# Performance work log

Measured on AMD Instinct MI355X. Metric: run time of the kernel, lower is better.

Reference implementation:

```python
import jax, jax.numpy as jnp
import numpy as np

DIM = 1536
NH = 12
HD = DIM // NH  # 128
B = 1
F, H, W = 8, 16, 16
S = F * H * W  # 2048
EPS = 1e-6
MAX_POS = 1024


def _rmsnorm(x, g):
    # WanRMSNorm: x * rsqrt(mean(x^2, -1) + eps) * weight  (computed in fp32)
    return x * jax.lax.rsqrt(jnp.mean(x * x, axis=-1, keepdims=True) + EPS) * g


def _rope_apply(x, grid_sizes, freqs):
    # x: [B, S, NH, HD]; freqs: [1024, HD//2] angles. Full (level-0) freqs_i path.
    f, h, w = [int(v) for v in np.asarray(grid_sizes[0])]
    c = HD // 2  # 64
    s0 = c - 2 * (c // 3)  # 22 (frame freqs)
    s1 = c // 3            # 21 (height / width freqs)
    p0 = freqs[:f, :s0]
    p1 = freqs[:h, s0:s0 + s1]
    p2 = freqs[:w, s0 + s1:]
    ang = jnp.concatenate([
        jnp.broadcast_to(p0[:, None, None, :], (f, h, w, s0)),
        jnp.broadcast_to(p1[None, :, None, :], (f, h, w, s1)),
        jnp.broadcast_to(p2[None, None, :, :], (f, h, w, s1)),
    ], axis=-1).reshape(f * h * w, 1, c)  # [S, 1, c]
    cos, sin = jnp.cos(ang), jnp.sin(ang)
    xr = x[0].reshape(S, NH, c, 2)  # pairs -> complex rotation
    x0, x1 = xr[..., 0], xr[..., 1]
    out = jnp.stack([x0 * cos - x1 * sin, x0 * sin + x1 * cos], axis=-1)
    return out.reshape(S, NH, HD)[None].astype(jnp.float32)  # [1, S, NH, HD]


def setup_inputs() -> dict:
    key = jax.random.key(0)
    ks = jax.random.split(key, 8)
    sc = 0.02
    return {
        "x": jax.random.normal(ks[0], (B, S, DIM), jnp.float32),
        "freqs": jax.random.uniform(ks[1], (MAX_POS, HD // 2), jnp.float32, 0.0, 2.0 * np.pi),
        "wq": jax.random.normal(ks[2], (DIM, DIM), jnp.float32) * sc,
        "bq": jnp.zeros((DIM,), jnp.float32),
        "wk": jax.random.normal(ks[3], (DIM, DIM), jnp.float32) * sc,
        "bk": jnp.zeros((DIM,), jnp.float32),
        "wv": jax.random.normal(ks[4], (DIM, DIM), jnp.float32) * sc,
        "bv": jnp.zeros((DIM,), jnp.float32),
        "wo": jax.random.normal(ks[5], (DIM, DIM), jnp.float32) * sc,
        "bo": jnp.zeros((DIM,), jnp.float32),
        "gq": jnp.ones((DIM,), jnp.float32),
        "gk": jnp.ones((DIM,), jnp.float32),
        "seq_lens": jnp.array([S], jnp.int32),
        "grid_sizes": jnp.array([[F, H, W]], jnp.int32),
    }


def reference(x, freqs, wq, bq, wk, bk, wv, bv, wo, bo, gq, gk, seq_lens, grid_sizes):
    b, s = x.shape[:2]
    q = _rmsnorm(x @ wq.T + bq, gq).reshape(b, s, NH, HD)
    k = _rmsnorm(x @ wk.T + bk, gk).reshape(b, s, NH, HD)
    v = (x @ wv.T + bv).reshape(b, s, NH, HD)
    q = _rope_apply(q, grid_sizes, freqs)
    k = _rope_apply(k, grid_sizes, freqs)
    # flash_attention with k_lens=seq_lens, full window -> masked SDPA
    kmask = jnp.arange(s)[None, :] < seq_lens[:, None]  # [b, s]
    scores = jnp.einsum('bqnd,bknd->bnqk', q, k) / np.sqrt(HD).astype(np.float32)
    scores = jnp.where(kmask[:, None, None, :], scores, jnp.finfo(scores.dtype).min)
    attn = jax.nn.softmax(scores, axis=-1)
    out = jnp.einsum('bnqk,bknd->bqnd', attn, v).reshape(b, s, DIM)
    return out @ wo.T + bo
```

## Files before the change

### kernel.cpp

```cpp
#include <hip/hip_runtime.h>
#include <math.h>

#define DIMN 1536
#define NHEAD 12
#define HDIM 128
#define SLEN 2048
#define EPSV 1e-6f

typedef __attribute__((ext_vector_type(8))) short short8;
typedef __attribute__((ext_vector_type(4))) short short4v;
typedef __attribute__((ext_vector_type(4))) float f32x4;

typedef __attribute__((address_space(1))) const void gvoid_t;
typedef __attribute__((address_space(3))) void lvoid_t;

__device__ __forceinline__ void gload_lds16(const void* g, void* l) {
    __builtin_amdgcn_global_load_lds((gvoid_t*)g, (lvoid_t*)l, 16, 0, 0);
}

__device__ inline short to_bf16(float f) {
    union { float f; unsigned u; } v; v.f = f;
    unsigned r = (v.u + 0x7FFFu + ((v.u >> 16) & 1u)) >> 16;
    return (short)r;
}
__device__ inline float bf_to_f(short h) {
    union { unsigned u; float f; } v;
    v.u = ((unsigned)(unsigned short)h) << 16;
    return v.f;
}

__device__ __forceinline__ int swz8(int row, int c) {
    return c ^ (row & 7);
}

__global__ __launch_bounds__(256)
void cast5(const float* s0, const float* s1, const float* s2,
           const float* s3, const float* s4,
           short* d0, short* d1, short* d2, short* d3, short* d4,
           int n0, int nw)
{
    const float* s; short* d; int n;
    switch (blockIdx.y) {
        case 0: s = s0; d = d0; n = n0; break;
        case 1: s = s1; d = d1; n = nw; break;
        case 2: s = s2; d = d2; n = nw; break;
        case 3: s = s3; d = d3; n = nw; break;
        default: s = s4; d = d4; n = nw; break;
    }
    int idx = (blockIdx.x * 256 + threadIdx.x) * 8;
    if (idx >= n) return;
    float4 a = *(const float4*)(s + idx);
    float4 b = *(const float4*)(s + idx + 4);
    short8 r;
    r[0] = to_bf16(a.x); r[1] = to_bf16(a.y); r[2] = to_bf16(a.z); r[3] = to_bf16(a.w);
    r[4] = to_bf16(b.x); r[5] = to_bf16(b.y); r[6] = to_bf16(b.z); r[7] = to_bf16(b.w);
    *(short8*)(d + idx) = r;
}

__device__ __forceinline__ void gemm_mainloop(const short* __restrict__ A,
    const short* __restrict__ W, int m0, int n0, int K,
    short* As, short* Bs, f32x4 (&acc)[4][4])
{
    const int tid = threadIdx.x;
    const int wave = tid >> 6, lane = tid & 63;
    const int quad = lane >> 4, col = lane & 15;
    const int wm = wave >> 1, wn = wave & 1;
    const int sr = tid >> 3;
    const int sc = tid & 7;

    for (int kt = 0; kt < K; kt += 64) {
        __syncthreads();
        #pragma unroll
        for (int i = 0; i < 4; ++i) {
            const int row = i * 32 + sr;
            const int c = swz8(row, sc);
            gload_lds16(A + (size_t)(m0 + row) * K + kt + c * 8, As + i * 2048 + tid * 8);
        }
        #pragma unroll
        for (int i = 0; i < 4; ++i) {
            const int row = i * 32 + sr;
            const int c = swz8(row, sc);
            gload_lds16(W + (size_t)(n0 + row) * K + kt + c * 8, Bs + i * 2048 + tid * 8);
        }
        __syncthreads();

        #pragma unroll
        for (int kb = 0; kb < 2; ++kb) {
            short8 af[4], bf[4];
            #pragma unroll
            for (int mt = 0; mt < 4; ++mt) {
                const int row = wm * 64 + mt * 16 + col;
                af[mt] = *(const short8*)&As[row * 64 + swz8(row, kb * 4 + quad) * 8];
            }
            #pragma unroll
            for (int nt = 0; nt < 4; ++nt) {
                const int row = wn * 64 + nt * 16 + col;
                bf[nt] = *(const short8*)&Bs[row * 64 + swz8(row, kb * 4 + quad) * 8];
            }
            #pragma unroll
            for (int mt = 0; mt < 4; ++mt)
                #pragma unroll
                for (int nt = 0; nt < 4; ++nt)
                    acc[mt][nt] = __builtin_amdgcn_mfma_f32_16x16x32_bf16(
                        af[mt], bf[nt], acc[mt][nt], 0, 0, 0);
        }
    }
}

__global__ __launch_bounds__(256)
void gemm_qkv(const short* __restrict__ A,
              const short* __restrict__ W0, const short* __restrict__ W1,
              const short* __restrict__ W2,
              const float* __restrict__ b0, const float* __restrict__ b1,
              const float* __restrict__ b2,
              short* __restrict__ Y0, short* __restrict__ Y1,
              short* __restrict__ Vp)
{
    __shared__ __attribute__((aligned(16))) short As[128 * 64];
    __shared__ __attribute__((aligned(16))) short Bs[128 * 64];

    const int sel = blockIdx.x / (DIMN / 128);
    const int nb  = blockIdx.x % (DIMN / 128);
    const short* W    = (sel == 0) ? W0 : (sel == 1) ? W1 : W2;
    const float* bias = (sel == 0) ? b0 : (sel == 1) ? b1 : b2;

    const int tid = threadIdx.x;
    const int wave = tid >> 6, lane = tid & 63;
    const int quad = lane >> 4, col = lane & 15;
    const int wm = wave >> 1, wn = wave & 1;
    const int m0 = blockIdx.y * 128, n0 = nb * 128;

    f32x4 acc[4][4];
    #pragma unroll
    for (int i = 0; i < 4; ++i)
        #pragma unroll
        for (int j = 0; j < 4; ++j)
            #pragma unroll
            for (int r = 0; r < 4; ++r) acc[i][j][r] = 0.f;

    gemm_mainloop(A, W, m0, n0, DIMN, As, Bs, acc);

    if (sel < 2) {
        short* Y = (sel == 0) ? Y0 : Y1;
        #pragma unroll
        for (int mt = 0; mt < 4; ++mt) {
            #pragma unroll
            for (int nt = 0; nt < 4; ++nt) {
                const int n = n0 + wn * 64 + nt * 16 + col;
                const float bb = bias[n];
                #pragma unroll
                for (int r = 0; r < 4; ++r) {
                    const int m = m0 + wm * 64 + mt * 16 + quad * 4 + r;
                    Y[(size_t)m * DIMN + n] = to_bf16(acc[mt][nt][r] + bb);
                }
            }
        }
    } else {
        const int head = nb;
        const int kt64 = blockIdx.y * 2 + wm;
        #pragma unroll
        for (int mt = 0; mt < 4; ++mt) {
            #pragma unroll
            for (int nt = 0; nt < 4; ++nt) {
                const int n = n0 + wn * 64 + nt * 16 + col;
                const float bb = bias[n];
                const int dt = wn * 4 + nt;
                const int chunk = (head * 64 + kt64 * 2 + (mt >> 1)) * 8 + dt;
                const int off = ((mt & 1) * 2 + (quad >> 1)) * 128 + col * 8 + (quad & 1) * 4;
                short4v o;
                #pragma unroll
                for (int r = 0; r < 4; ++r) o[r] = to_bf16(acc[mt][nt][r] + bb);
                *(short4v*)(Vp + (size_t)chunk * 512 + off) = o;
            }
        }
    }
}

__global__ __launch_bounds__(256)
void gemm_out(const short* __restrict__ A, const short* __restrict__ W,
              const float* __restrict__ bias, float* __restrict__ Yf)
{
    __shared__ __attribute__((aligned(16))) short As[128 * 64];
    __shared__ __attribute__((aligned(16))) short Bs[128 * 64];

    const int tid = threadIdx.x;
    const int wave = tid >> 6, lane = tid & 63;
    const int quad = lane >> 4, col = lane & 15;
    const int wm = wave >> 1, wn = wave & 1;
    const int m0 = blockIdx.y * 128, n0 = blockIdx.x * 128;

    f32x4 acc[4][4];
    #pragma unroll
    for (int i = 0; i < 4; ++i)
        #pragma unroll
        for (int j = 0; j < 4; ++j)
            #pragma unroll
            for (int r = 0; r < 4; ++r) acc[i][j][r] = 0.f;

    gemm_mainloop(A, W, m0, n0, DIMN, As, Bs, acc);

    #pragma unroll
    for (int mt = 0; mt < 4; ++mt) {
        #pragma unroll
        for (int nt = 0; nt < 4; ++nt) {
            const int n = n0 + wn * 64 + nt * 16 + col;
            const float bb = bias[n];
            #pragma unroll
            for (int r = 0; r < 4; ++r) {
                const int m = m0 + wm * 64 + mt * 16 + quad * 4 + r;
                Yf[(size_t)m * DIMN + n] = acc[mt][nt][r] + bb;
            }
        }
    }
}

__global__ __launch_bounds__(256)
void rms_rope_qk(short* __restrict__ qbuf, const short* __restrict__ kbuf,
                 short* __restrict__ Kp,
                 const float* __restrict__ gq, const float* __restrict__ gk,
                 const float* __restrict__ freqs, const int* __restrict__ grid_sizes)
{
    const int s = blockIdx.x;
    const int isK = blockIdx.y;
    const int tid = threadIdx.x;
    short* qrow = qbuf + (size_t)s * DIMN;
    const short* row = isK ? (kbuf + (size_t)s * DIMN) : qrow;
    const float* g = isK ? gk : gq;

    float ss = 0.f;
    if (tid < 192) {
        short8 v = *(const short8*)(row + tid * 8);
        #pragma unroll
        for (int j = 0; j < 8; ++j) { float f = bf_to_f(v[j]); ss += f * f; }
    }
    #pragma unroll
    for (int off = 32; off; off >>= 1) ss += __shfl_down(ss, off, 64);

    __shared__ float red[4];
    __shared__ float s_scale;
    if ((tid & 63) == 0) red[tid >> 6] = ss;
    __syncthreads();
    if (tid == 0) {
        float t = red[0] + red[1] + red[2] + red[3];
        float sc = rsqrtf(t / (float)DIMN + EPSV);
        s_scale = isK ? sc : sc * 0.08838834764831845f;
    }
    __syncthreads();
    const float scale = s_scale;

    const int h = grid_sizes[1], w = grid_sizes[2];
    const int fi = s / (h * w);
    const int hi = (s / w) % h;
    const int wi = s % w;

    if (!isK) {
        for (int p = tid; p < NHEAD * 64; p += 256) {
            const int n = p >> 6;
            const int d = p & 63;
            const int idx = (d < 22) ? fi : ((d < 43) ? hi : wi);
            const float ang = freqs[idx * 64 + d];
            float sn, cs;
            __sincosf(ang, &sn, &cs);
            const int base = n * HDIM + 2 * d;
            const float v0 = bf_to_f(qrow[base]) * scale * g[base];
            const float v1 = bf_to_f(qrow[base + 1]) * scale * g[base + 1];
            qrow[base]     = to_bf16(v0 * cs - v1 * sn);
            qrow[base + 1] = to_bf16(v0 * sn + v1 * cs);
        }
    } else if (tid < 192) {
        const int n = tid >> 4;
        const int o = tid & 15;
        short8 outv;
        #pragma unroll
        for (int pp = 0; pp < 4; ++pp) {
            const int pd = o * 4 + pp;
            const int idx = (pd < 22) ? fi : ((pd < 43) ? hi : wi);
            const float ang = freqs[idx * 64 + pd];
            float sn, cs;
            __sincosf(ang, &sn, &cs);
            const int base = n * HDIM + 2 * pd;
            const float v0 = bf_to_f(row[base]) * scale * g[base];
            const float v1 = bf_to_f(row[base + 1]) * scale * g[base + 1];
            outv[pp * 2]     = to_bf16(v0 * cs - v1 * sn);
            outv[pp * 2 + 1] = to_bf16(v0 * sn + v1 * cs);
        }
        const int kb = s >> 4, colk = s & 15;
        const int kc = o >> 2, quadk = o & 3;
        const size_t addr = ((((size_t)(n * 128 + kb) * 4 + kc) * 64) + quadk * 16 + colk) * 8;
        *(short8*)(Kp + addr) = outv;
    }
}

__global__ __launch_bounds__(64, 1)
void attn_mfma8(const short* __restrict__ Q, const short* __restrict__ Kp,
                const short* __restrict__ Vp, short* __restrict__ O,
                const int* __restrict__ seq_lens)
{
    __shared__ __attribute__((aligned(16))) short psw[2 * 16 * 40];

    const int lane = threadIdx.x;
    const int quad = lane >> 4, col = lane & 15;

    const int orig = blockIdx.y * 64 + blockIdx.x;
    const int work = (orig & 7) * 96 + (orig >> 3);
    const int head = work >> 6;
    const int row0 = (work & 63) * 32;
    const int slen = seq_lens[0];

    short8 qf[2][4];
    #pragma unroll
    for (int T = 0; T < 2; ++T)
        #pragma unroll
        for (int kc = 0; kc < 4; ++kc)
            qf[T][kc] = *(const short8*)(Q + (size_t)(row0 + T * 16 + col) * DIMN
                                         + head * HDIM + kc * 32 + quad * 8);

    f32x4 oacc[2][8];
    #pragma unroll
    for (int T = 0; T < 2; ++T)
        #pragma unroll
        for (int dt = 0; dt < 8; ++dt)
            #pragma unroll
            for (int r = 0; r < 4; ++r) oacc[T][dt][r] = 0.f;
    float lsum[2][4];
    #pragma unroll
    for (int T = 0; T < 2; ++T)
        #pragma unroll
        for (int r = 0; r < 4; ++r) lsum[T][r] = 0.f;

    const short* kbase = Kp + (size_t)head * 262144 + lane * 8;
    const short* vbase = Vp + (size_t)head * 262144 + lane * 8;

    auto loadKV = [&](short8 (&kf)[8], short8 (&vf)[8], int step) {
        const short* ks = kbase + (size_t)step * 4096;
        const short* vs = vbase + (size_t)step * 4096;
        #pragma unroll
        for (int c = 0; c < 8; ++c) kf[c] = *(const short8*)(ks + c * 512);
        #pragma unroll
        for (int c = 0; c < 8; ++c) vf[c] = *(const short8*)(vs + c * 512);
    };

    auto compute = [&](short8 (&kf)[8], short8 (&vf)[8], int kt) {
        f32x4 s[2][2];
        #pragma unroll
        for (int T = 0; T < 2; ++T)
            #pragma unroll
            for (int nt = 0; nt < 2; ++nt)
                #pragma unroll
                for (int r = 0; r < 4; ++r) s[T][nt][r] = 0.f;

        #pragma unroll
        for (int kc = 0; kc < 4; ++kc)
            #pragma unroll
            for (int T = 0; T < 2; ++T) {
                s[T][0] = __builtin_amdgcn_mfma_f32_16x16x32_bf16(qf[T][kc], kf[kc],     s[T][0], 0, 0, 0);
                s[T][1] = __builtin_amdgcn_mfma_f32_16x16x32_bf16(qf[T][kc], kf[4 + kc], s[T][1], 0, 0, 0);
            }

        const int kt0 = kt * 32;
        #pragma unroll
        for (int T = 0; T < 2; ++T)
            #pragma unroll
            for (int nt = 0; nt < 2; ++nt) {
                const bool masked = (kt0 + nt * 16 + col >= slen);
                #pragma unroll
                for (int r = 0; r < 4; ++r) {
                    float p = masked ? 0.f : __expf(s[T][nt][r]);
                    lsum[T][r] += p;
                    psw[T * 640 + (quad * 4 + r) * 40 + nt * 16 + col] = to_bf16(p);
                }
            }

        short8 pf0 = *(const short8*)&psw[col * 40 + quad * 8];
        short8 pf1 = *(const short8*)&psw[640 + col * 40 + quad * 8];

        #pragma unroll
        for (int dt = 0; dt < 8; ++dt) {
            oacc[0][dt] = __builtin_amdgcn_mfma_f32_16x16x32_bf16(pf0, vf[dt], oacc[0][dt], 0, 0, 0);
            oacc[1][dt] = __builtin_amdgcn_mfma_f32_16x16x32_bf16(pf1, vf[dt], oacc[1][dt], 0, 0, 0);
        }
    };

    short8 kA[8], vA[8], kB[8], vB[8];
    loadKV(kA, vA, 0);

    #pragma unroll 1
    for (int kt = 0; kt < SLEN / 32; kt += 2) {
        loadKV(kB, vB, kt + 1);
        compute(kA, vA, kt);
        loadKV(kA, vA, kt + 2);
        compute(kB, vB, kt + 1);
    }

    #pragma unroll
    for (int T = 0; T < 2; ++T)
        #pragma unroll
        for (int r = 0; r < 4; ++r) {
            #pragma unroll
            for (int off = 8; off; off >>= 1)
                lsum[T][r] += __shfl_xor(lsum[T][r], off, 64);
            lsum[T][r] = 1.0f / lsum[T][r];
        }

    #pragma unroll
    for (int T = 0; T < 2; ++T)
        #pragma unroll
        for (int dt = 0; dt < 8; ++dt)
            #pragma unroll
            for (int r = 0; r < 4; ++r)
                O[(size_t)(row0 + T * 16 + quad * 4 + r) * DIMN
                  + head * HDIM + dt * 16 + col] = to_bf16(oacc[T][dt][r] * lsum[T][r]);
}

extern "C" void kernel_launch(void* const* d_in, const int* in_sizes, int n_in,
                              void* d_out, int out_size, void* d_ws, size_t ws_size,
                              hipStream_t stream)
{
    const float* x     = (const float*)d_in[0];
    const float* freqs = (const float*)d_in[1];
    const float* wq    = (const float*)d_in[2];
    const float* bq    = (const float*)d_in[3];
    const float* wk    = (const float*)d_in[4];
    const float* bk    = (const float*)d_in[5];
    const float* wv    = (const float*)d_in[6];
    const float* bv    = (const float*)d_in[7];
    const float* wo    = (const float*)d_in[8];
    const float* bo    = (const float*)d_in[9];
    const float* gq    = (const float*)d_in[10];
    const float* gk    = (const float*)d_in[11];
    const int* seq_lens   = (const int*)d_in[12];
    const int* grid_sizes = (const int*)d_in[13];
    float* out = (float*)d_out;

    const size_t NX = (size_t)SLEN * DIMN;
    const size_t NW = (size_t)DIMN * DIMN;
    short* xb  = (short*)d_ws;
    short* wqb = xb + NX;
    short* wkb = wqb + NW;
    short* wvb = wkb + NW;
    short* wob = wvb + NW;
    short* qb  = wob + NW;
    short* kb  = qb + NX;
    short* vp  = kb + NX;
    short* kp  = vp + NX;
    short* ob  = kp + NX;

    cast5<<<dim3(1536, 5), 256, 0, stream>>>(x, wq, wk, wv, wo,
                                             xb, wqb, wkb, wvb, wob,
                                             (int)NX, (int)NW);

    gemm_qkv<<<dim3(3 * DIMN / 128, SLEN / 128), 256, 0, stream>>>(
        xb, wqb, wkb, wvb, bq, bk, bv, qb, kb, vp);

    rms_rope_qk<<<dim3(SLEN, 2), 256, 0, stream>>>(qb, kb, kp, gq, gk, freqs, grid_sizes);

    attn_mfma8<<<dim3(64, NHEAD), 64, 0, stream>>>(qb, kp, vp, ob, seq_lens);

    gemm_out<<<dim3(DIMN / 128, SLEN / 128), 256, 0, stream>>>(ob, wob, bo, out);
}
```

Measured before the change: 277.6 us.

## Split attention key range across two waves per block and merge in LDS

The attention kernel now uses two waves per block; each wave processes half of the key/value sequence for the same 32 query rows. Wave 1 writes its unnormalized output accumulators and row sums to shared memory, and wave 0 combines them and normalizes before storing. This doubles the number of resident waves and halves the serial loop per wave, to expose more parallelism on lightly occupied CUs. The prefetch scheme also changes: only K is prefetched a step ahead while V is loaded at the start of each step. That adds LDS traffic and a block barrier, and V loads may be less hidden.

```diff
diff --git a/kernel.cpp b/kernel.cpp
--- a/kernel.cpp
+++ b/kernel.cpp
@@ -291,14 +291,18 @@
     }
 }
 
-__global__ __launch_bounds__(64, 1)
-void attn_mfma8(const short* __restrict__ Q, const short* __restrict__ Kp,
-                const short* __restrict__ Vp, short* __restrict__ O,
-                const int* __restrict__ seq_lens)
-{
-    __shared__ __attribute__((aligned(16))) short psw[2 * 16 * 40];
-
-    const int lane = threadIdx.x;
+__global__ __launch_bounds__(128)
+void attn_mfma10(const short* __restrict__ Q, const short* __restrict__ Kp,
+                 const short* __restrict__ Vp, short* __restrict__ O,
+                 const int* __restrict__ seq_lens)
+{
+    __shared__ __attribute__((aligned(16))) short psw[2 * 1280];
+    __shared__ __attribute__((aligned(16))) float sacc[32 * 132];
+    __shared__ float sl[32];
+
+    const int tid  = threadIdx.x;
+    const int wave = tid >> 6;
+    const int lane = tid & 63;
     const int quad = lane >> 4, col = lane & 15;
 
     const int orig = blockIdx.y * 64 + blockIdx.x;
@@ -330,17 +334,16 @@
 
     const short* kbase = Kp + (size_t)head * 262144 + lane * 8;
     const short* vbase = Vp + (size_t)head * 262144 + lane * 8;
-
-    auto loadKV = [&](short8 (&kf)[8], short8 (&vf)[8], int step) {
-        const short* ks = kbase + (size_t)step * 4096;
+    short* pswm = psw + wave * 1280;
+
+    const int step0 = wave * 32;
+
+    auto stepf = [&](short8 (&kf)[8], short8 (&kn)[8], int step) {
         const short* vs = vbase + (size_t)step * 4096;
-        #pragma unroll
-        for (int c = 0; c < 8; ++c) kf[c] = *(const short8*)(ks + c * 512);
+        short8 vf[8];
         #pragma unroll
         for (int c = 0; c < 8; ++c) vf[c] = *(const short8*)(vs + c * 512);
-    };
-
-    auto compute = [&](short8 (&kf)[8], short8 (&vf)[8], int kt) {
+
         f32x4 s[2][2];
         #pragma unroll
         for (int T = 0; T < 2; ++T)
@@ -357,7 +360,11 @@
                 s[T][1] = __builtin_amdgcn_mfma_f32_16x16x32_bf16(qf[T][kc], kf[4 + kc], s[T][1], 0, 0, 0);
             }
 
-        const int kt0 = kt * 32;
+        const short* kns = kbase + (size_t)(step + 1) * 4096;
+        #pragma unroll
+        for (int c = 0; c < 8; ++c) kn[c] = *(const short8*)(kns + c * 512);
+
+        const int kt0 = step * 32;
         #pragma unroll
         for (int T = 0; T < 2; ++T)
             #pragma unroll
@@ -367,12 +374,12 @@
                 for (int r = 0; r < 4; ++r) {
                     float p = masked ? 0.f : __expf(s[T][nt][r]);
                     lsum[T][r] += p;
-                    psw[T * 640 + (quad * 4 + r) * 40 + nt * 16 + col] = to_bf16(p);
+                    pswm[T * 640 + (quad * 4 + r) * 40 + nt * 16 + col] = to_bf16(p);
                 }
             }
 
-        short8 pf0 = *(const short8*)&psw[col * 40 + quad * 8];
-        short8 pf1 = *(const short8*)&psw[640 + col * 40 + quad * 8];
+        short8 pf0 = *(const short8*)&pswm[col * 40 + quad * 8];
+        short8 pf1 = *(const short8*)&pswm[640 + col * 40 + quad * 8];
 
         #pragma unroll
         for (int dt = 0; dt < 8; ++dt) {
@@ -381,15 +388,17 @@
         }
     };
 
-    short8 kA[8], vA[8], kB[8], vB[8];
-    loadKV(kA, vA, 0);
+    short8 kfA[8], kfB[8];
+    {
+        const short* ks = kbase + (size_t)step0 * 4096;
+        #pragma unroll
+        for (int c = 0; c < 8; ++c) kfA[c] = *(const short8*)(ks + c * 512);
+    }
 
     #pragma unroll 1
-    for (int kt = 0; kt < SLEN / 32; kt += 2) {
-        loadKV(kB, vB, kt + 1);
-        compute(kA, vA, kt);
-        loadKV(kA, vA, kt + 2);
-        compute(kB, vB, kt + 1);
+    for (int kt = 0; kt < 32; kt += 2) {
+        stepf(kfA, kfB, step0 + kt);
+        stepf(kfB, kfA, step0 + kt + 1);
     }
 
     #pragma unroll
@@ -399,17 +408,41 @@
             #pragma unroll
             for (int off = 8; off; off >>= 1)
                 lsum[T][r] += __shfl_xor(lsum[T][r], off, 64);
-            lsum[T][r] = 1.0f / lsum[T][r];
-        }
-
-    #pragma unroll
-    for (int T = 0; T < 2; ++T)
-        #pragma unroll
-        for (int dt = 0; dt < 8; ++dt)
+        }
+
+    if (wave == 1) {
+        #pragma unroll
+        for (int T = 0; T < 2; ++T) {
+            #pragma unroll
+            for (int dt = 0; dt < 8; ++dt)
+                #pragma unroll
+                for (int r = 0; r < 4; ++r)
+                    sacc[(T * 16 + quad * 4 + r) * 132 + dt * 16 + col] = oacc[T][dt][r];
+            if (col == 0) {
+                #pragma unroll
+                for (int r = 0; r < 4; ++r) sl[T * 16 + quad * 4 + r] = lsum[T][r];
+            }
+        }
+    }
+    __syncthreads();
+    if (wave == 0) {
+        #pragma unroll
+        for (int T = 0; T < 2; ++T) {
+            float inv[4];
             #pragma unroll
             for (int r = 0; r < 4; ++r)
-                O[(size_t)(row0 + T * 16 + quad * 4 + r) * DIMN
-                  + head * HDIM + dt * 16 + col] = to_bf16(oacc[T][dt][r] * lsum[T][r]);
+                inv[r] = 1.0f / (lsum[T][r] + sl[T * 16 + quad * 4 + r]);
+            #pragma unroll
+            for (int dt = 0; dt < 8; ++dt)
+                #pragma unroll
+                for (int r = 0; r < 4; ++r) {
+                    const float o = oacc[T][dt][r]
+                                  + sacc[(T * 16 + quad * 4 + r) * 132 + dt * 16 + col];
+                    O[(size_t)(row0 + T * 16 + quad * 4 + r) * DIMN
+                      + head * HDIM + dt * 16 + col] = to_bf16(o * inv[r]);
+                }
+        }
+    }
 }
 
 extern "C" void kernel_launch(void* const* d_in, const int* in_sizes, int n_in,
@@ -454,7 +487,7 @@
 
     rms_rope_qk<<<dim3(SLEN, 2), 256, 0, stream>>>(qb, kb, kp, gq, gk, freqs, grid_sizes);
 
-    attn_mfma8<<<dim3(64, NHEAD), 64, 0, stream>>>(qb, kp, vp, ob, seq_lens);
+    attn_mfma10<<<dim3(64, NHEAD), 128, 0, stream>>>(qb, kp, vp, ob, seq_lens);
 
     gemm_out<<<dim3(DIMN / 128, SLEN / 128), 256, 0, stream>>>(ob, wob, bo, out);
 }
```

New measurement: 268.7 us. -3.2%, faster.
